# Optimization experiments

Measured on AMD Instinct MI355X. Metric: run time of the kernel, lower is better.

## Reference

```python
import jax, jax.numpy as jnp
import numpy as np

NB = 256  # images are quantized to 256 intensity levels (uint8 pipeline)


def _histograms(q):
    # q: int32 (BC, N) values in [0, NB)
    BC, N = q.shape
    idx = (q + jnp.arange(BC, dtype=jnp.int32)[:, None] * NB).reshape(-1)
    ones = jnp.ones((BC * N,), dtype=jnp.int32)
    return jax.ops.segment_sum(ones, idx, num_segments=BC * NB).reshape(BC, NB)


def _match_lut(counts_s, counts_r):
    # Fixed-shape emulation of the per-channel np.unique/cumsum/np.interp loop.
    occ_s = counts_s > 0
    occ_r = counts_r > 0
    first_s = jnp.argmax(occ_s)  # smallest unique source value (dropped, maps to 0)
    first_r = jnp.argmax(occ_r)  # smallest unique reference value (dropped)
    cs = counts_s.at[first_s].set(0)
    cr = counts_r.at[first_r].set(0)
    cums = jnp.cumsum(cs).astype(jnp.float32)
    cumr = jnp.cumsum(cr).astype(jnp.float32)
    s_q = cums / jnp.maximum(cums[-1], 1.0)  # source quantiles at every bin
    r_q = cumr / jnp.maximum(cumr[-1], 1.0)
    # Compact occupied reference bins (excluding the first) to the front so that
    # jnp.interp sees only the quantiles/values that np.unique would produce.
    occ_r2 = occ_r & (jnp.arange(NB) != first_r)
    order = jnp.argsort(jnp.logical_not(occ_r2))  # stable: occupied bins first, ascending
    occ_sorted = occ_r2[order]
    xp = jnp.where(occ_sorted, r_q[order], 2.0)   # pad with x>1 so queries (<=1) never reach pads
    fp = jnp.where(occ_sorted, order.astype(jnp.float32), 0.0)
    lut = jnp.trunc(jnp.interp(s_q, xp, fp))  # trunc == C-style cast into uint8 result buffer
    lut = lut.at[first_s].set(0.0)            # interp_value[0] = 0 in the original
    ok = (jnp.sum(occ_s) > 1) & (jnp.sum(occ_r) > 1)  # 'continue' branch -> zeros
    return jnp.where(ok, lut, 0.0)


def _match_histogram(source, reference):
    # source/reference: float (B,3,H,W) with values at exact 0..255 levels
    B, C, H, W = source.shape
    sq = jnp.clip(jnp.round(source), 0, NB - 1).astype(jnp.int32).reshape(B * C, H * W)
    rq = jnp.clip(jnp.round(reference), 0, NB - 1).astype(jnp.int32).reshape(B * C, H * W)
    lut = jax.vmap(_match_lut)(_histograms(sq), _histograms(rq))  # (BC, NB)
    return jnp.take_along_axis(lut, sq, axis=1).reshape(B, C, H, W)


def reference(input_data, target_data, ref_data, mask_src, mask_tar):
    to_img = lambda x: (x + 1.0) * 0.5 * 255.0  # tensor2image(x) * 255
    inp = to_img(input_data)
    tar = to_img(target_data)
    ref = to_img(ref_data)
    m_src = jnp.broadcast_to(mask_src, inp.shape)
    m_tar = jnp.broadcast_to(mask_tar, tar.shape)
    input_masked = inp * m_src
    target_masked = tar * m_tar
    ref_masked = ref * m_src
    matched = jax.lax.stop_gradient(_match_histogram(ref_masked, target_masked))
    input_match = matched * m_src
    return jnp.mean(jnp.abs(input_masked - input_match))  # L1Loss


def setup_inputs() -> dict:
    key = jax.random.key(0)
    k1, k2, k3, k4, k5 = jax.random.split(key, 5)
    B, H, W = 8, 512, 512

    def img(k):
        # exact multiples of 1/255 in [-1,1] -> integer 0..255 after tensor2image*255
        levels = jax.random.randint(k, (B, 3, H, W), 0, 256).astype(jnp.float32)
        return (levels / 255.0) * 2.0 - 1.0

    def mask(k):
        return (jax.random.uniform(k, (B, 1, H, W)) > 0.3).astype(jnp.float32)

    return {
        "input_data": img(k1),
        "target_data": img(k2),
        "ref_data": img(k3),
        "mask_src": mask(k4),
        "mask_tar": mask(k5),
    }
```

## Files before the change

### kernel.cpp

```cpp
#include <hip/hip_runtime.h>
#include <hip/hip_bf16.h>

#define HW    262144
#define HW4   65536
#define BC    24
#define NB    256
#define NTOT  6291456

#define GH    64
#define GL    64

#define WS_HS_OFF   0
#define WS_HR_OFF   24576
#define WS_ACC_OFF  49152
#define WS_LUT_OFF  49216
#define WS_ZERO_BYTES 49156

__device__ __forceinline__ int quantize(float x, float m) {
    float v = (x + 1.0f) * 0.5f * 255.0f * m;
    float r = rintf(v);
    r = fminf(fmaxf(r, 0.0f), 255.0f);
    return (int)r;
}

__device__ __forceinline__ int incl_scan256(int v, int t, int* buf) {
    buf[t] = v;
    __syncthreads();
#pragma unroll
    for (int off = 1; off < NB; off <<= 1) {
        int x = (t >= off) ? buf[t - off] : 0;
        __syncthreads();
        buf[t] += x;
        __syncthreads();
    }
    return buf[t];
}

__global__ void hist_kernel(const float4* __restrict__ ref4,
                            const float4* __restrict__ tar4,
                            const float4* __restrict__ ms4,
                            const float4* __restrict__ mt4,
                            int* __restrict__ hs, int* __restrict__ hr) {
    __shared__ int wh[4 * 2 * NB];
    const int t = threadIdx.x;
    const int wave = t >> 6;
    const int lane = t & 63;
#pragma unroll
    for (int j = 0; j < 8; ++j) wh[t + j * 256] = 0;
    __syncthreads();

    const int c = blockIdx.y;
    const int b = c / 3;
    const float4* refc = ref4 + (size_t)c * HW4;
    const float4* tarc = tar4 + (size_t)c * HW4;
    const float4* msb  = ms4 + (size_t)b * HW4;
    const float4* mtb  = mt4 + (size_t)b * HW4;

    int* whS = &wh[wave * 512];
    int* whR = &wh[wave * 512 + 256];
    int n0s = 0, n0r = 0;

    for (int i = blockIdx.x * blockDim.x + t; i < HW4; i += GH * 256) {
        const float4 r  = refc[i];
        const float4 m  = msb[i];
        const float4 tv = tarc[i];
        const float4 mm = mtb[i];

        const float rv[4]  = {r.x, r.y, r.z, r.w};
        const float mv[4]  = {m.x, m.y, m.z, m.w};
        const float tvv[4] = {tv.x, tv.y, tv.z, tv.w};
        const float mtv[4] = {mm.x, mm.y, mm.z, mm.w};
#pragma unroll
        for (int k = 0; k < 4; ++k) {
            if (mv[k] != 0.0f) atomicAdd(&whS[quantize(rv[k], mv[k])], 1);
            else n0s++;
            if (mtv[k] != 0.0f) atomicAdd(&whR[quantize(tvv[k], mtv[k])], 1);
            else n0r++;
        }
    }
#pragma unroll
    for (int off = 32; off > 0; off >>= 1) {
        n0s += __shfl_down(n0s, off);
        n0r += __shfl_down(n0r, off);
    }
    if (lane == 0) {
        if (n0s) atomicAdd(&whS[0], n0s);
        if (n0r) atomicAdd(&whR[0], n0r);
    }
    __syncthreads();

    const int s = wh[t] + wh[512 + t] + wh[1024 + t] + wh[1536 + t];
    const int r = wh[256 + t] + wh[768 + t] + wh[1280 + t] + wh[1792 + t];
    if (s) atomicAdd(&hs[c * NB + t], s);
    if (r) atomicAdd(&hr[c * NB + t], r);
}

__global__ void lut_kernel(const int* __restrict__ hs,
                           const int* __restrict__ hr,
                           float* __restrict__ lut) {
    const int c = blockIdx.x;
    const int t = threadIdx.x;

    __shared__ int buf[NB];
    __shared__ float xp[NB];
    __shared__ float fp[NB];
    __shared__ int firstS, firstR, nOccS, nOccR;

    const int cs = hs[c * NB + t];
    const int cr = hr[c * NB + t];

    if (t == 0) { firstS = NB; firstR = NB; nOccS = 0; nOccR = 0; }
    __syncthreads();
    if (cs > 0) { atomicMin(&firstS, t); atomicAdd(&nOccS, 1); }
    if (cr > 0) { atomicMin(&firstR, t); atomicAdd(&nOccR, 1); }
    __syncthreads();

    const int csz = (t == firstS) ? 0 : cs;
    const int crz = (t == firstR) ? 0 : cr;

    const int cumS = incl_scan256(csz, t, buf);
    const int totS = buf[NB - 1];
    __syncthreads();
    const int cumR = incl_scan256(crz, t, buf);
    const int totR = buf[NB - 1];
    __syncthreads();
    const int occ2 = (cr > 0 && t != firstR) ? 1 : 0;
    const int rank = incl_scan256(occ2, t, buf) - occ2;
    __syncthreads();

    const float x  = (float)cumS / fmaxf((float)totS, 1.0f);
    const float rq = (float)cumR / fmaxf((float)totR, 1.0f);

    xp[t] = 2.0f;
    fp[t] = 0.0f;
    __syncthreads();
    if (occ2) { xp[rank] = rq; fp[rank] = (float)t; }
    __syncthreads();

    int lo = 0, hi = NB;
    while (lo < hi) {
        int mid = (lo + hi) >> 1;
        if (xp[mid] > x) hi = mid; else lo = mid + 1;
    }
    int i = lo;
    i = (i < 1) ? 1 : ((i > NB - 1) ? NB - 1 : i);
    float dxv = xp[i] - xp[i - 1];
    float f;
    if (dxv == 0.0f) f = fp[i];
    else f = fp[i - 1] + (x - xp[i - 1]) / dxv * (fp[i] - fp[i - 1]);
    if (x < xp[0]) f = fp[0];

    float l = truncf(f);
    if (t == firstS) l = 0.0f;
    if (!((nOccS > 1) && (nOccR > 1))) l = 0.0f;

    lut[c * NB + t] = l;
}

__global__ void loss_kernel(const float4* __restrict__ inp4,
                            const float4* __restrict__ ref4,
                            const float4* __restrict__ ms4,
                            const float* __restrict__ lut,
                            float* __restrict__ accum) {
    __shared__ float llut[NB];
    const int t = threadIdx.x;
    const int c = blockIdx.y;
    const int b = c / 3;
    llut[t] = lut[c * NB + t];
    __syncthreads();

    const float4* inpc = inp4 + (size_t)c * HW4;
    const float4* refc = ref4 + (size_t)c * HW4;
    const float4* msb  = ms4 + (size_t)b * HW4;

    float s = 0.0f;
    for (int i = blockIdx.x * blockDim.x + t; i < HW4; i += GL * 256) {
        const float4 x = inpc[i];
        const float4 r = refc[i];
        const float4 m = msb[i];
        const float xv[4] = {x.x, x.y, x.z, x.w};
        const float rv[4] = {r.x, r.y, r.z, r.w};
        const float mv[4] = {m.x, m.y, m.z, m.w};
#pragma unroll
        for (int k = 0; k < 4; ++k) {
            if (mv[k] != 0.0f) {
                const int q = quantize(rv[k], mv[k]);
                const float im = (xv[k] + 1.0f) * 127.5f;
                s += fabsf(im - llut[q]);
            }
        }
    }

#pragma unroll
    for (int off = 32; off > 0; off >>= 1) s += __shfl_down(s, off);
    __shared__ float wsum[4];
    const int lane = t & 63;
    const int wave = t >> 6;
    if (lane == 0) wsum[wave] = s;
    __syncthreads();
    if (t == 0) atomicAdd(accum, wsum[0] + wsum[1] + wsum[2] + wsum[3]);
}

__global__ void finalize_kernel(const float* __restrict__ accum,
                                float* __restrict__ out) {
    out[0] = accum[0] / (float)NTOT;
}

extern "C" void kernel_launch(void* const* d_in, const int* in_sizes, int n_in,
                              void* d_out, int out_size, void* d_ws, size_t ws_size,
                              hipStream_t stream) {
    const float* inp  = (const float*)d_in[0];
    const float* tar  = (const float*)d_in[1];
    const float* ref  = (const float*)d_in[2];
    const float* msrc = (const float*)d_in[3];
    const float* mtar = (const float*)d_in[4];

    char* ws = (char*)d_ws;
    int*   hs    = (int*)(ws + WS_HS_OFF);
    int*   hr    = (int*)(ws + WS_HR_OFF);
    float* accum = (float*)(ws + WS_ACC_OFF);
    float* lut   = (float*)(ws + WS_LUT_OFF);

    hipMemsetAsync(d_ws, 0, WS_ZERO_BYTES, stream);

    hist_kernel<<<dim3(GH, BC), 256, 0, stream>>>(
        (const float4*)ref, (const float4*)tar,
        (const float4*)msrc, (const float4*)mtar, hs, hr);

    lut_kernel<<<BC, 256, 0, stream>>>(hs, hr, lut);

    loss_kernel<<<dim3(GL, BC), 256, 0, stream>>>(
        (const float4*)inp, (const float4*)ref, (const float4*)msrc,
        lut, accum);

    finalize_kernel<<<1, 1, 0, stream>>>(accum, (float*)d_out);
}
```

Baseline: 150.8 us.

## Replace global atomics with per-block partial histograms and sums, preload loads upfront

```diff
diff --git a/kernel.cpp b/kernel.cpp
--- a/kernel.cpp
+++ b/kernel.cpp
@@ -10,11 +10,10 @@
 #define GH    64
 #define GL    64
 
-#define WS_HS_OFF   0
-#define WS_HR_OFF   24576
-#define WS_ACC_OFF  49152
-#define WS_LUT_OFF  49216
-#define WS_ZERO_BYTES 49156
+#define WS_HSP_OFF  0
+#define WS_HRP_OFF  1572864
+#define WS_LSUM_OFF 3145728
+#define WS_LUT_OFF  3151872
 
 __device__ __forceinline__ int quantize(float x, float m) {
     float v = (x + 1.0f) * 0.5f * 255.0f * m;
@@ -36,11 +35,12 @@
     return buf[t];
 }
 
-__global__ void hist_kernel(const float4* __restrict__ ref4,
-                            const float4* __restrict__ tar4,
-                            const float4* __restrict__ ms4,
-                            const float4* __restrict__ mt4,
-                            int* __restrict__ hs, int* __restrict__ hr) {
+__global__ void __launch_bounds__(256)
+hist_kernel(const float4* __restrict__ ref4,
+            const float4* __restrict__ tar4,
+            const float4* __restrict__ ms4,
+            const float4* __restrict__ mt4,
+            int* __restrict__ hsPart, int* __restrict__ hrPart) {
     __shared__ int wh[4 * 2 * NB];
     const int t = threadIdx.x;
     const int wave = t >> 6;
@@ -56,20 +56,27 @@
     const float4* msb  = ms4 + (size_t)b * HW4;
     const float4* mtb  = mt4 + (size_t)b * HW4;
 
+    const int base = blockIdx.x * 256 + t;
+
+    float4 R[4], T[4], M[4], MT[4];
+#pragma unroll
+    for (int j = 0; j < 4; ++j) R[j]  = refc[base + j * 16384];
+#pragma unroll
+    for (int j = 0; j < 4; ++j) M[j]  = msb[base + j * 16384];
+#pragma unroll
+    for (int j = 0; j < 4; ++j) T[j]  = tarc[base + j * 16384];
+#pragma unroll
+    for (int j = 0; j < 4; ++j) MT[j] = mtb[base + j * 16384];
+
     int* whS = &wh[wave * 512];
     int* whR = &wh[wave * 512 + 256];
     int n0s = 0, n0r = 0;
-
-    for (int i = blockIdx.x * blockDim.x + t; i < HW4; i += GH * 256) {
-        const float4 r  = refc[i];
-        const float4 m  = msb[i];
-        const float4 tv = tarc[i];
-        const float4 mm = mtb[i];
-
-        const float rv[4]  = {r.x, r.y, r.z, r.w};
-        const float mv[4]  = {m.x, m.y, m.z, m.w};
-        const float tvv[4] = {tv.x, tv.y, tv.z, tv.w};
-        const float mtv[4] = {mm.x, mm.y, mm.z, mm.w};
+#pragma unroll
+    for (int j = 0; j < 4; ++j) {
+        const float rv[4]  = {R[j].x, R[j].y, R[j].z, R[j].w};
+        const float mv[4]  = {M[j].x, M[j].y, M[j].z, M[j].w};
+        const float tvv[4] = {T[j].x, T[j].y, T[j].z, T[j].w};
+        const float mtv[4] = {MT[j].x, MT[j].y, MT[j].z, MT[j].w};
 #pragma unroll
         for (int k = 0; k < 4; ++k) {
             if (mv[k] != 0.0f) atomicAdd(&whS[quantize(rv[k], mv[k])], 1);
@@ -91,13 +98,14 @@
 
     const int s = wh[t] + wh[512 + t] + wh[1024 + t] + wh[1536 + t];
     const int r = wh[256 + t] + wh[768 + t] + wh[1280 + t] + wh[1792 + t];
-    if (s) atomicAdd(&hs[c * NB + t], s);
-    if (r) atomicAdd(&hr[c * NB + t], r);
-}
-
-__global__ void lut_kernel(const int* __restrict__ hs,
-                           const int* __restrict__ hr,
-                           float* __restrict__ lut) {
+    hsPart[(c * GH + blockIdx.x) * NB + t] = s;
+    hrPart[(c * GH + blockIdx.x) * NB + t] = r;
+}
+
+__global__ void __launch_bounds__(256)
+lut_kernel(const int* __restrict__ hsPart,
+           const int* __restrict__ hrPart,
+           float* __restrict__ lut) {
     const int c = blockIdx.x;
     const int t = threadIdx.x;
 
@@ -106,8 +114,12 @@
     __shared__ float fp[NB];
     __shared__ int firstS, firstR, nOccS, nOccR;
 
-    const int cs = hs[c * NB + t];
-    const int cr = hr[c * NB + t];
+    int cs = 0, cr = 0;
+#pragma unroll 4
+    for (int g = 0; g < GH; ++g) {
+        cs += hsPart[(c * GH + g) * NB + t];
+        cr += hrPart[(c * GH + g) * NB + t];
+    }
 
     if (t == 0) { firstS = NB; firstR = NB; nOccS = 0; nOccR = 0; }
     __syncthreads();
@@ -157,11 +169,12 @@
     lut[c * NB + t] = l;
 }
 
-__global__ void loss_kernel(const float4* __restrict__ inp4,
-                            const float4* __restrict__ ref4,
-                            const float4* __restrict__ ms4,
-                            const float* __restrict__ lut,
-                            float* __restrict__ accum) {
+__global__ void __launch_bounds__(256)
+loss_kernel(const float4* __restrict__ inp4,
+            const float4* __restrict__ ref4,
+            const float4* __restrict__ ms4,
+            const float* __restrict__ lut,
+            float* __restrict__ lsum) {
     __shared__ float llut[NB];
     const int t = threadIdx.x;
     const int c = blockIdx.y;
@@ -173,21 +186,27 @@
     const float4* refc = ref4 + (size_t)c * HW4;
     const float4* msb  = ms4 + (size_t)b * HW4;
 
+    const int base = blockIdx.x * 256 + t;
+
+    float4 X[4], R[4], M[4];
+#pragma unroll
+    for (int j = 0; j < 4; ++j) X[j] = inpc[base + j * 16384];
+#pragma unroll
+    for (int j = 0; j < 4; ++j) R[j] = refc[base + j * 16384];
+#pragma unroll
+    for (int j = 0; j < 4; ++j) M[j] = msb[base + j * 16384];
+
     float s = 0.0f;
-    for (int i = blockIdx.x * blockDim.x + t; i < HW4; i += GL * 256) {
-        const float4 x = inpc[i];
-        const float4 r = refc[i];
-        const float4 m = msb[i];
-        const float xv[4] = {x.x, x.y, x.z, x.w};
-        const float rv[4] = {r.x, r.y, r.z, r.w};
-        const float mv[4] = {m.x, m.y, m.z, m.w};
+#pragma unroll
+    for (int j = 0; j < 4; ++j) {
+        const float xv[4] = {X[j].x, X[j].y, X[j].z, X[j].w};
+        const float rv[4] = {R[j].x, R[j].y, R[j].z, R[j].w};
+        const float mv[4] = {M[j].x, M[j].y, M[j].z, M[j].w};
 #pragma unroll
         for (int k = 0; k < 4; ++k) {
-            if (mv[k] != 0.0f) {
-                const int q = quantize(rv[k], mv[k]);
-                const float im = (xv[k] + 1.0f) * 127.5f;
-                s += fabsf(im - llut[q]);
-            }
+            const int q = quantize(rv[k], mv[k]);
+            const float im = (xv[k] + 1.0f) * 127.5f;
+            s += mv[k] * fabsf(im - llut[q]);
         }
     }
 
@@ -198,12 +217,25 @@
     const int wave = t >> 6;
     if (lane == 0) wsum[wave] = s;
     __syncthreads();
-    if (t == 0) atomicAdd(accum, wsum[0] + wsum[1] + wsum[2] + wsum[3]);
-}
-
-__global__ void finalize_kernel(const float* __restrict__ accum,
-                                float* __restrict__ out) {
-    out[0] = accum[0] / (float)NTOT;
+    if (t == 0)
+        lsum[c * GL + blockIdx.x] = wsum[0] + wsum[1] + wsum[2] + wsum[3];
+}
+
+__global__ void __launch_bounds__(256)
+finalize_kernel(const float* __restrict__ lsum, float* __restrict__ out) {
+    const int t = threadIdx.x;
+    float s = 0.0f;
+#pragma unroll
+    for (int i = t; i < BC * GL; i += 256) s += lsum[i];
+#pragma unroll
+    for (int off = 32; off > 0; off >>= 1) s += __shfl_down(s, off);
+    __shared__ float wsum[4];
+    const int lane = t & 63;
+    const int wave = t >> 6;
+    if (lane == 0) wsum[wave] = s;
+    __syncthreads();
+    if (t == 0)
+        out[0] = (wsum[0] + wsum[1] + wsum[2] + wsum[3]) / (float)NTOT;
 }
 
 extern "C" void kernel_launch(void* const* d_in, const int* in_sizes, int n_in,
@@ -216,22 +248,20 @@
     const float* mtar = (const float*)d_in[4];
 
     char* ws = (char*)d_ws;
-    int*   hs    = (int*)(ws + WS_HS_OFF);
-    int*   hr    = (int*)(ws + WS_HR_OFF);
-    float* accum = (float*)(ws + WS_ACC_OFF);
-    float* lut   = (float*)(ws + WS_LUT_OFF);
-
-    hipMemsetAsync(d_ws, 0, WS_ZERO_BYTES, stream);
+    int*   hsPart = (int*)(ws + WS_HSP_OFF);
+    int*   hrPart = (int*)(ws + WS_HRP_OFF);
+    float* lsum   = (float*)(ws + WS_LSUM_OFF);
+    float* lut    = (float*)(ws + WS_LUT_OFF);
 
     hist_kernel<<<dim3(GH, BC), 256, 0, stream>>>(
         (const float4*)ref, (const float4*)tar,
-        (const float4*)msrc, (const float4*)mtar, hs, hr);
-
-    lut_kernel<<<BC, 256, 0, stream>>>(hs, hr, lut);
+        (const float4*)msrc, (const float4*)mtar, hsPart, hrPart);
+
+    lut_kernel<<<BC, 256, 0, stream>>>(hsPart, hrPart, lut);
 
     loss_kernel<<<dim3(GL, BC), 256, 0, stream>>>(
         (const float4*)inp, (const float4*)ref, (const float4*)msrc,
-        lut, accum);
-
-    finalize_kernel<<<1, 1, 0, stream>>>(accum, (float*)d_out);
-}
+        lut, lsum);
+
+    finalize_kernel<<<1, 256, 0, stream>>>(lsum, (float*)d_out);
+}
```

Measured after the change: 137.3 us. 9.0% less time.
